# Kernel optimization log

Measured on AMD Instinct MI355X. Metric: run time of the kernel, lower is better.

## Reference

```python
import jax, jax.numpy as jnp
import numpy as np

N = 50000      # nodes
E = 800000     # edges (before self-loops)
H = 2          # attention heads
C = 64         # hidden_channels (per-head out since concat=False)
L = 3          # num_layers - 2 conv blocks
OUT = 128      # readout out_channels
G = 512        # num graphs
VOCAB = 100    # embedding table size
NEG_SLOPE = 0.2


def setup_inputs() -> dict:
    key = jax.random.key(0)
    ks = jax.random.split(key, 12)
    s = 1.0 / np.sqrt(C)
    x = jax.random.randint(ks[0], (N,), 0, VOCAB, dtype=jnp.int32)
    edge_index = jax.random.randint(ks[1], (2, E), 0, N, dtype=jnp.int32)
    batch = jnp.sort(jax.random.randint(ks[2], (N,), 0, G, dtype=jnp.int32))
    embed = jax.random.normal(ks[3], (VOCAB, C), dtype=jnp.float32) * s
    lin_W = jax.random.normal(ks[4], (L, C, C), dtype=jnp.float32) * s
    lin_b = jnp.zeros((L, C), dtype=jnp.float32)
    gat_Wl = jax.random.normal(ks[5], (L, C, H * C), dtype=jnp.float32) * s
    gat_bl = jnp.zeros((L, H * C), dtype=jnp.float32)
    gat_Wr = jax.random.normal(ks[6], (L, C, H * C), dtype=jnp.float32) * s
    gat_br = jnp.zeros((L, H * C), dtype=jnp.float32)
    gat_att = jax.random.normal(ks[7], (L, H, C), dtype=jnp.float32) * s
    gat_bias = jnp.zeros((L, C), dtype=jnp.float32)
    readout_W = jax.random.normal(ks[8], (C, OUT), dtype=jnp.float32) * s
    readout_b = jnp.zeros((OUT,), dtype=jnp.float32)
    return {"x": x, "edge_index": edge_index, "batch": batch, "num_graphs": G,
            "embed": embed, "lin_W": lin_W, "lin_b": lin_b,
            "gat_Wl": gat_Wl, "gat_bl": gat_bl, "gat_Wr": gat_Wr, "gat_br": gat_br,
            "gat_att": gat_att, "gat_bias": gat_bias,
            "readout_W": readout_W, "readout_b": readout_b}


def _gatv2_layer(h, src, dst, Wl, bl, Wr, br, att, bias):
    # lin_l -> source/message features, lin_r -> target features (PyG GATv2Conv)
    xl = (h @ Wl + bl).reshape(N, H, C)
    xr = (h @ Wr + br).reshape(N, H, C)
    # per-edge GATv2 score: a^T LeakyReLU(x_l[j] + x_r[i])
    e = jax.nn.leaky_relu(xl[src] + xr[dst], NEG_SLOPE)      # [E2,H,C]
    score = jnp.einsum('ehc,hc->eh', e, att)                 # [E2,H]
    # segment softmax over incoming edges of each dst node (stable)
    m = jax.lax.stop_gradient(jax.ops.segment_max(score, dst, num_segments=N))
    p = jnp.exp(score - m[dst])
    denom = jax.ops.segment_sum(p, dst, num_segments=N)      # [N,H]
    alpha = p / denom[dst]                                   # [E2,H]
    msg = xl[src] * alpha[:, :, None]                        # [E2,H,C]
    agg = jax.ops.segment_sum(msg, dst, num_segments=N)      # [N,H,C]
    return agg.mean(axis=1) + bias                           # concat=False -> head mean


def reference(x, edge_index, batch, num_graphs, embed, lin_W, lin_b,
              gat_Wl, gat_bl, gat_Wr, gat_br, gat_att, gat_bias,
              readout_W, readout_b):
    # add self loops (GATv2Conv default add_self_loops=True)
    loops = jnp.arange(N, dtype=edge_index.dtype)
    src = jnp.concatenate([edge_index[0], loops])
    dst = jnp.concatenate([edge_index[1], loops])
    h = embed[x]                                             # [N,C]
    for l in range(L):
        h = jax.nn.relu(h @ lin_W[l] + lin_b[l])             # dropout is a no-op in eval
        h = _gatv2_layer(h, src, dst, gat_Wl[l], gat_bl[l], gat_Wr[l], gat_br[l],
                         gat_att[l], gat_bias[l])
    out = h @ readout_W + readout_b                          # [N,OUT]
    return jax.ops.segment_sum(out, batch, num_segments=num_graphs)  # [G,OUT]
```

## Files before the change

### kernel.cpp

```cpp
#include <hip/hip_runtime.h>
#include <hip/hip_fp16.h>

#define N_NODES  50000
#define E_EDGES  800000
#define E_TOT    850000
#define H_HEADS  2
#define C_DIM    64
#define HC       128
#define L_LAYERS 3
#define OUT_DIM  128
#define G_GRAPHS 512
#define NEG_SLOPE 0.2f
#define SCAN_B   196

typedef float v2f __attribute__((ext_vector_type(2)));

__device__ __forceinline__ void lds_fence() { asm volatile("" ::: "memory"); }

__global__ void embed_kernel(const int* __restrict__ x, const float* __restrict__ embed,
                             float* __restrict__ h, int* __restrict__ counts) {
    int i = blockIdx.x * 256 + threadIdx.x;
    if (i < N_NODES) counts[i] = 0;
    if (i >= N_NODES * C_DIM) return;
    int n = i >> 6, c = i & 63;
    h[i] = embed[x[n] * C_DIM + c];
}

__global__ void csr_count_kernel(const int* __restrict__ dsts, int* __restrict__ counts) {
    int e = blockIdx.x * 256 + threadIdx.x;
    if (e >= E_TOT) return;
    int d = (e < E_EDGES) ? dsts[e] : e - E_EDGES;
    atomicAdd(&counts[d], 1);
}

__global__ void scan_partial_kernel(const int* __restrict__ counts, int* __restrict__ row_ptr,
                                    int* __restrict__ partials) {
    __shared__ int wsum[4];
    int i = blockIdx.x * 256 + threadIdx.x;
    int lane = threadIdx.x & 63, wid = threadIdx.x >> 6;
    int cnt = (i < N_NODES) ? counts[i] : 0;
    int v = cnt;
#pragma unroll
    for (int off = 1; off < 64; off <<= 1) {
        int t = __shfl_up(v, off, 64);
        if (lane >= off) v += t;
    }
    if (lane == 63) wsum[wid] = v;
    __syncthreads();
    int woff = 0;
#pragma unroll
    for (int w = 0; w < 4; w++) if (w < wid) woff += wsum[w];
    v += woff;
    if (i < N_NODES) row_ptr[i] = v - cnt;
    if (threadIdx.x == 255) partials[blockIdx.x] = v;
}

__global__ void scan_offsets_kernel(const int* __restrict__ partials, int* __restrict__ block_off) {
    __shared__ int wsum[4];
    int tid = threadIdx.x;
    int lane = tid & 63, wid = tid >> 6;
    int cnt = (tid < SCAN_B) ? partials[tid] : 0;
    int v = cnt;
#pragma unroll
    for (int off = 1; off < 64; off <<= 1) {
        int t = __shfl_up(v, off, 64);
        if (lane >= off) v += t;
    }
    if (lane == 63) wsum[wid] = v;
    __syncthreads();
    int woff = 0;
#pragma unroll
    for (int w = 0; w < 4; w++) if (w < wid) woff += wsum[w];
    v += woff;
    if (tid < SCAN_B) block_off[tid] = v - cnt;
}

__global__ void scan_add_kernel(int* __restrict__ row_ptr, const int* __restrict__ block_off,
                                int* __restrict__ write_off) {
    int i = blockIdx.x * 256 + threadIdx.x;
    if (i < N_NODES) {
        int v = row_ptr[i] + block_off[blockIdx.x];
        row_ptr[i] = v;
        write_off[i] = v;
    }
    if (i == 0) row_ptr[N_NODES] = E_TOT;
}

__global__ void csr_scatter_kernel(const int* __restrict__ srcs, const int* __restrict__ dsts,
                                   int* __restrict__ write_off, int* __restrict__ src_sorted) {
    int e = blockIdx.x * 256 + threadIdx.x;
    if (e >= E_TOT) return;
    int s, d;
    if (e < E_EDGES) { s = srcs[e]; d = dsts[e]; }
    else             { s = d = e - E_EDGES; }
    int pos = atomicAdd(&write_off[d], 1);
    src_sorted[pos] = s;
}

__global__ void layer_lin_kernel(const float* __restrict__ h,
                                 const float* __restrict__ W, const float* __restrict__ b,
                                 const float* __restrict__ Wl, const float* __restrict__ bl,
                                 const float* __restrict__ Wr, const float* __restrict__ br,
                                 __half* __restrict__ xlh, float* __restrict__ xri) {
    __shared__ float sH[16 * 64];
    __shared__ float sH2[16 * 64];
    int tid = threadIdx.x;
    int base = blockIdx.x * 16;
#pragma unroll
    for (int i = 0; i < 4; i++) {
        int idx = tid + i * 256;
        int nn = base + (idx >> 6);
        sH[idx] = (nn < N_NODES) ? h[(size_t)nn * 64 + (idx & 63)] : 0.f;
    }
    __syncthreads();
    {
        int c = tid & 63, g = tid >> 6;
        float a0 = b[c], a1 = a0, a2 = a0, a3 = a0;
        for (int k = 0; k < 64; k++) {
            float wv = W[k * 64 + c];
            a0 = fmaf(sH[(g * 4 + 0) * 64 + k], wv, a0);
            a1 = fmaf(sH[(g * 4 + 1) * 64 + k], wv, a1);
            a2 = fmaf(sH[(g * 4 + 2) * 64 + k], wv, a2);
            a3 = fmaf(sH[(g * 4 + 3) * 64 + k], wv, a3);
        }
        sH2[(g * 4 + 0) * 64 + c] = fmaxf(a0, 0.f);
        sH2[(g * 4 + 1) * 64 + c] = fmaxf(a1, 0.f);
        sH2[(g * 4 + 2) * 64 + c] = fmaxf(a2, 0.f);
        sH2[(g * 4 + 3) * 64 + c] = fmaxf(a3, 0.f);
    }
    __syncthreads();
    {
        int j = tid & 127, gg = tid >> 7;
        float accl[8], accr[8];
#pragma unroll
        for (int n = 0; n < 8; n++) { accl[n] = bl[j]; accr[n] = br[j]; }
        for (int k = 0; k < 64; k++) {
            float wl = Wl[k * 128 + j], wr = Wr[k * 128 + j];
#pragma unroll
            for (int n = 0; n < 8; n++) {
                float hv = sH2[(gg * 8 + n) * 64 + k];
                accl[n] = fmaf(hv, wl, accl[n]);
                accr[n] = fmaf(hv, wr, accr[n]);
            }
        }
        int hh = j >> 6, c = j & 63;
#pragma unroll
        for (int n = 0; n < 8; n++) {
            int node = base + gg * 8 + n;
            if (node < N_NODES) {
                size_t o = (size_t)node * 128 + c * 2 + hh;
                xlh[o] = __float2half(accl[n]);
                xri[o] = accr[n];
            }
        }
    }
}

__global__ void gat_kernel(const __half2* __restrict__ xlh, const float2* __restrict__ xr2,
                           const float* __restrict__ att, const int* __restrict__ row_ptr,
                           const int* __restrict__ src_sorted, const float* __restrict__ bias,
                           float* __restrict__ h_out) {
    __shared__ __align__(16) float cbuf[4][8 * 132];
    int w = threadIdx.x >> 6;
    int d = blockIdx.x * 4 + w;
    if (d >= N_NODES) return;
    int lane = threadIdx.x & 63;
    int r0 = row_ptr[d], r1 = row_ptr[d + 1];
    float2 vrf = xr2[(size_t)d * 64 + lane];
    v2f vr2 = {vrf.x, vrf.y};
    v2f att2 = {att[lane], att[64 + lane]};
    float* cb = cbuf[w];
    int e_of = lane >> 3, p = lane & 7;

    float dpx = 0.f, dpy = 0.f;
    v2f ac0 = {0.f, 0.f}, ac1 = {0.f, 0.f};

#define GAT_LOAD(V, CB) do {                                                    \
        int lim_ = nchunk - 1;                                                  \
        _Pragma("unroll")                                                       \
        for (int e = 0; e < 8; e++) {                                           \
            int ee_ = (CB) + e;                                                 \
            int sv_ = __builtin_amdgcn_readlane(idx, (ee_ < nchunk) ? ee_ : lim_); \
            V[e] = xlh[(size_t)sv_ * 64 + lane];                                \
        }                                                                       \
    } while (0)

#define GAT_PROC(V, CB) do {                                                    \
        int rem_ = nchunk - (CB);                                               \
        v2f vf8[8];                                                             \
        _Pragma("unroll")                                                       \
        for (int e = 0; e < 8; e++) {                                           \
            float2 vf_ = __half22float2(V[e]);                                  \
            v2f vl2 = {vf_.x, vf_.y};                                           \
            vf8[e] = vl2;                                                       \
            v2f z = vl2 + vr2;                                                  \
            v2f t = __builtin_elementwise_max(z, z * NEG_SLOPE) * att2;         \
            *(v2f*)&cb[e * 132 + 2 * lane] = t;                                 \
        }                                                                       \
        lds_fence();                                                            \
        v2f s2 = {0.f, 0.f};                                                    \
        {                                                                       \
            const float4* row_ = (const float4*)&cb[e_of * 132 + p * 16];       \
            _Pragma("unroll")                                                   \
            for (int j = 0; j < 4; j++) {                                       \
                float4 f = row_[j];                                             \
                s2 += (v2f){f.x, f.y};                                          \
                s2 += (v2f){f.z, f.w};                                          \
            }                                                                   \
        }                                                                       \
        lds_fence();                                                            \
        _Pragma("unroll")                                                       \
        for (int off = 1; off <= 4; off <<= 1) {                                \
            v2f o_;                                                             \
            o_.x = __shfl_xor(s2.x, off, 64);                                   \
            o_.y = __shfl_xor(s2.y, off, 64);                                   \
            s2 += o_;                                                           \
        }                                                                       \
        float sx = s2.x, sy = s2.y;                                             \
        if (e_of >= rem_) { sx = -INFINITY; sy = -INFINITY; }                   \
        float wx = __expf(sx), wy = __expf(sy);                                 \
        dpx += wx; dpy += wy;                                                   \
        _Pragma("unroll")                                                       \
        for (int e = 0; e < 8; e++) {                                           \
            float swx = __int_as_float(__builtin_amdgcn_readlane(__float_as_int(wx), 8 * e)); \
            float swy = __int_as_float(__builtin_amdgcn_readlane(__float_as_int(wy), 8 * e)); \
            v2f w2 = {swx, swy};                                                \
            if (e & 1) ac1 = __builtin_elementwise_fma(w2, vf8[e], ac1);        \
            else       ac0 = __builtin_elementwise_fma(w2, vf8[e], ac0);        \
        }                                                                       \
    } while (0)

    for (int base = r0; base < r1; base += 64) {
        int a = base + lane;
        int idx = src_sorted[(a < r1) ? a : (r1 - 1)];
        int nchunk = min(64, r1 - base);
        __half2 va[8], vb[8];
        GAT_LOAD(va, 0);
        int cb_i = 0;
        for (;;) {
            int nx = cb_i + 8;
            if (nx < nchunk) {
                GAT_LOAD(vb, nx);
                GAT_PROC(va, cb_i);
                cb_i = nx;
            } else {
                GAT_PROC(va, cb_i);
                break;
            }
            nx = cb_i + 8;
            if (nx < nchunk) {
                GAT_LOAD(va, nx);
                GAT_PROC(vb, cb_i);
                cb_i = nx;
            } else {
                GAT_PROC(vb, cb_i);
                break;
            }
        }
    }
#undef GAT_LOAD
#undef GAT_PROC

#pragma unroll
    for (int off = 8; off <= 32; off <<= 1) {
        dpx += __shfl_xor(dpx, off, 64);
        dpy += __shfl_xor(dpy, off, 64);
    }
    v2f acc = ac0 + ac1;
    h_out[(size_t)d * 64 + lane] = (acc.x / dpx + acc.y / dpy) * 0.5f + bias[lane];
}

__global__ void zero_out_kernel(float* __restrict__ out) {
    int i = blockIdx.x * 256 + threadIdx.x;
    if (i < G_GRAPHS * OUT_DIM) out[i] = 0.f;
}

__global__ void readout_kernel(const float* __restrict__ h, const float* __restrict__ W,
                               const float* __restrict__ b, const int* __restrict__ batch,
                               float* __restrict__ out) {
    __shared__ float sH[16 * 64];
    __shared__ int sB[16];
    int tid = threadIdx.x;
    int base = blockIdx.x * 16;
#pragma unroll
    for (int i = 0; i < 4; i++) {
        int idx = tid + i * 256;
        int nn = base + (idx >> 6);
        sH[idx] = (nn < N_NODES) ? h[(size_t)nn * 64 + (idx & 63)] : 0.f;
    }
    if (tid < 16) sB[tid] = (base + tid < N_NODES) ? batch[base + tid] : -1;
    __syncthreads();
    int j = tid & 127, gg = tid >> 7;
    float acc[8];
#pragma unroll
    for (int n = 0; n < 8; n++) acc[n] = b[j];
    for (int k = 0; k < 64; k++) {
        float wv = W[k * OUT_DIM + j];
#pragma unroll
        for (int n = 0; n < 8; n++) acc[n] = fmaf(sH[(gg * 8 + n) * 64 + k], wv, acc[n]);
    }
    float run = 0.f; int curb = -2;
#pragma unroll
    for (int n = 0; n < 8; n++) {
        int node = base + gg * 8 + n;
        int bb = (node < N_NODES) ? sB[gg * 8 + n] : -1;
        if (bb != curb) {
            if (curb >= 0) atomicAdd(&out[curb * OUT_DIM + j], run);
            run = 0.f; curb = bb;
        }
        if (bb >= 0) run += acc[n];
    }
    if (curb >= 0) atomicAdd(&out[curb * OUT_DIM + j], run);
}

extern "C" void kernel_launch(void* const* d_in, const int* in_sizes, int n_in,
                              void* d_out, int out_size, void* d_ws, size_t ws_size,
                              hipStream_t stream) {
    const int*   x        = (const int*)d_in[0];
    const int*   edge     = (const int*)d_in[1];
    const int*   batch    = (const int*)d_in[2];
    const float* embed    = (const float*)d_in[4];
    const float* lin_W    = (const float*)d_in[5];
    const float* lin_b    = (const float*)d_in[6];
    const float* gat_Wl   = (const float*)d_in[7];
    const float* gat_bl   = (const float*)d_in[8];
    const float* gat_Wr   = (const float*)d_in[9];
    const float* gat_br   = (const float*)d_in[10];
    const float* gat_att  = (const float*)d_in[11];
    const float* gat_bias = (const float*)d_in[12];
    const float* ro_W     = (const float*)d_in[13];
    const float* ro_b     = (const float*)d_in[14];
    float* out = (float*)d_out;

    const int* srcs = edge;
    const int* dsts = edge + E_EDGES;

    float* h   = (float*)d_ws;
    __half* xlh = (__half*)(h + (size_t)N_NODES * 64);
    float* xr  = (float*)((char*)xlh + (size_t)N_NODES * HC * sizeof(__half));
    int* counts     = (int*)(xr + (size_t)N_NODES * HC);
    int* row_ptr    = counts + N_NODES;
    int* write_off  = row_ptr + N_NODES + 1;
    int* src_sorted = write_off + N_NODES;
    int* partials   = src_sorted + E_TOT;
    int* block_off  = partials + SCAN_B;

    const int T = 256;
    const int gEmbed = (N_NODES * C_DIM + 255) / 256;
    const int gEdge  = (E_TOT + 255) / 256;
    const int gLin   = (N_NODES + 15) / 16;
    const int gGat   = (N_NODES + 3) / 4;
    const int gOut   = (G_GRAPHS * OUT_DIM + 255) / 256;

    embed_kernel<<<gEmbed, T, 0, stream>>>(x, embed, h, counts);

    csr_count_kernel<<<gEdge, T, 0, stream>>>(dsts, counts);
    scan_partial_kernel<<<SCAN_B, T, 0, stream>>>(counts, row_ptr, partials);
    scan_offsets_kernel<<<1, T, 0, stream>>>(partials, block_off);
    scan_add_kernel<<<SCAN_B, T, 0, stream>>>(row_ptr, block_off, write_off);
    csr_scatter_kernel<<<gEdge, T, 0, stream>>>(srcs, dsts, write_off, src_sorted);

    for (int l = 0; l < L_LAYERS; l++) {
        layer_lin_kernel<<<gLin, T, 0, stream>>>(
            h,
            lin_W + (size_t)l * 64 * 64, lin_b + (size_t)l * 64,
            gat_Wl + (size_t)l * 64 * 128, gat_bl + (size_t)l * 128,
            gat_Wr + (size_t)l * 64 * 128, gat_br + (size_t)l * 128,
            xlh, xr);
        gat_kernel<<<gGat, T, 0, stream>>>(
            (const __half2*)xlh, (const float2*)xr, gat_att + (size_t)l * HC,
            row_ptr, src_sorted, gat_bias + (size_t)l * 64, h);
    }

    zero_out_kernel<<<gOut, T, 0, stream>>>(out);
    readout_kernel<<<gLin, T, 0, stream>>>(h, ro_W, ro_b, batch, out);
}
```

Measured before the change: 478.6 us.

## Build CSR via two-pass bucket partition and store sources as 16-bit indices

Replaces the per-edge global atomic scatter into CSR with a two-pass scheme. First, edges are partitioned into 196 buckets of 256 destination nodes using shared-memory histograms and one global atomic per bucket per block. Then each bucket is sorted locally into CSR order with shared atomics. Source indices are stored as unsigned short to halve index traffic in the GAT kernel, but node ids reach 49999 and only fit because that is below 65536; any larger graph would break it. The intent is to cut global atomic contention and scattered writes, at the cost of an extra kernel and an intermediate buffer.

```diff
diff --git a/kernel.cpp b/kernel.cpp
--- a/kernel.cpp
+++ b/kernel.cpp
@@ -12,6 +12,8 @@
 #define G_GRAPHS 512
 #define NEG_SLOPE 0.2f
 #define SCAN_B   196
+#define NB       196
+#define EPB      4096
 
 typedef float v2f __attribute__((ext_vector_type(2)));
 
@@ -76,25 +78,97 @@
 }
 
 __global__ void scan_add_kernel(int* __restrict__ row_ptr, const int* __restrict__ block_off,
-                                int* __restrict__ write_off) {
+                                int* __restrict__ bwptr) {
     int i = blockIdx.x * 256 + threadIdx.x;
     if (i < N_NODES) {
         int v = row_ptr[i] + block_off[blockIdx.x];
         row_ptr[i] = v;
-        write_off[i] = v;
+        if ((i & 255) == 0) bwptr[i >> 8] = v;
     }
     if (i == 0) row_ptr[N_NODES] = E_TOT;
 }
 
-__global__ void csr_scatter_kernel(const int* __restrict__ srcs, const int* __restrict__ dsts,
-                                   int* __restrict__ write_off, int* __restrict__ src_sorted) {
-    int e = blockIdx.x * 256 + threadIdx.x;
-    if (e >= E_TOT) return;
-    int s, d;
-    if (e < E_EDGES) { s = srcs[e]; d = dsts[e]; }
-    else             { s = d = e - E_EDGES; }
-    int pos = atomicAdd(&write_off[d], 1);
-    src_sorted[pos] = s;
+__global__ void edge_partition_kernel(const int* __restrict__ srcs, const int* __restrict__ dsts,
+                                      int* __restrict__ bwptr, unsigned int* __restrict__ ebuf) {
+    __shared__ int hist[256];
+    __shared__ int lscan[256];
+    __shared__ int sExcl[256];
+    __shared__ int lcnt[256];
+    __shared__ int gbase[256];
+    __shared__ unsigned int sval[EPB];
+    __shared__ unsigned char sgid[EPB];
+    int tid = threadIdx.x;
+    int ebase = blockIdx.x * EPB;
+    hist[tid] = 0;
+    __syncthreads();
+    unsigned int val[16];
+    int gid[16];
+#pragma unroll
+    for (int i = 0; i < 16; i++) {
+        int e = ebase + i * 256 + tid;
+        if (e < E_TOT) {
+            int s, d;
+            if (e < E_EDGES) { s = srcs[e]; d = dsts[e]; }
+            else             { s = d = e - E_EDGES; }
+            val[i] = ((unsigned)s << 8) | (unsigned)(d & 255);
+            gid[i] = d >> 8;
+            atomicAdd(&hist[gid[i]], 1);
+        } else gid[i] = -1;
+    }
+    __syncthreads();
+    lscan[tid] = hist[tid];
+    __syncthreads();
+#pragma unroll
+    for (int off = 1; off < 256; off <<= 1) {
+        int t = (tid >= off) ? lscan[tid - off] : 0;
+        __syncthreads();
+        lscan[tid] += t;
+        __syncthreads();
+    }
+    sExcl[tid] = lscan[tid] - hist[tid];
+    lcnt[tid] = 0;
+    __syncthreads();
+#pragma unroll
+    for (int i = 0; i < 16; i++) {
+        if (gid[i] >= 0) {
+            int off = atomicAdd(&lcnt[gid[i]], 1);
+            int idx = sExcl[gid[i]] + off;
+            sval[idx] = val[i];
+            sgid[idx] = (unsigned char)gid[i];
+        }
+    }
+    if (tid < NB) {
+        int c = hist[tid];
+        gbase[tid] = c ? atomicAdd(&bwptr[tid], c) : 0;
+    }
+    __syncthreads();
+    int total = lscan[255];
+    for (int idx = tid; idx < total; idx += 256) {
+        int g = sgid[idx];
+        ebuf[gbase[g] + (idx - sExcl[g])] = sval[idx];
+    }
+}
+
+__global__ void bucket_csr_kernel(const unsigned int* __restrict__ ebuf,
+                                  const int* __restrict__ row_ptr,
+                                  unsigned short* __restrict__ src_sorted) {
+    __shared__ int lbase[256];
+    __shared__ int lcnt[256];
+    int g = blockIdx.x, tid = threadIdx.x;
+    int n0 = g << 8;
+    int nodes = min(256, N_NODES - n0);
+    int b0 = row_ptr[n0];
+    int b1 = row_ptr[min(n0 + 256, N_NODES)];
+    if (tid < nodes) lbase[tid] = row_ptr[n0 + tid] - b0;
+    lcnt[tid] = 0;
+    __syncthreads();
+    int cnt = b1 - b0;
+    for (int i = tid; i < cnt; i += 256) {
+        unsigned int v = ebuf[b0 + i];
+        int dl = v & 255;
+        int slot = lbase[dl] + atomicAdd(&lcnt[dl], 1);
+        src_sorted[b0 + slot] = (unsigned short)(v >> 8);
+    }
 }
 
 __global__ void layer_lin_kernel(const float* __restrict__ h,
@@ -158,7 +232,8 @@
 
 __global__ void gat_kernel(const __half2* __restrict__ xlh, const float2* __restrict__ xr2,
                            const float* __restrict__ att, const int* __restrict__ row_ptr,
-                           const int* __restrict__ src_sorted, const float* __restrict__ bias,
+                           const unsigned short* __restrict__ src_sorted,
+                           const float* __restrict__ bias,
                            float* __restrict__ h_out) {
     __shared__ __align__(16) float cbuf[4][8 * 132];
     int w = threadIdx.x >> 6;
@@ -232,7 +307,7 @@
 
     for (int base = r0; base < r1; base += 64) {
         int a = base + lane;
-        int idx = src_sorted[(a < r1) ? a : (r1 - 1)];
+        int idx = (int)src_sorted[(a < r1) ? a : (r1 - 1)];
         int nchunk = min(64, r1 - base);
         __half2 va[8], vb[8];
         GAT_LOAD(va, 0);
@@ -335,19 +410,21 @@
     const int* srcs = edge;
     const int* dsts = edge + E_EDGES;
 
-    float* h   = (float*)d_ws;
+    float* h    = (float*)d_ws;
     __half* xlh = (__half*)(h + (size_t)N_NODES * 64);
-    float* xr  = (float*)((char*)xlh + (size_t)N_NODES * HC * sizeof(__half));
+    float* xr   = (float*)((char*)xlh + (size_t)N_NODES * HC * sizeof(__half));
     int* counts     = (int*)(xr + (size_t)N_NODES * HC);
     int* row_ptr    = counts + N_NODES;
-    int* write_off  = row_ptr + N_NODES + 1;
-    int* src_sorted = write_off + N_NODES;
-    int* partials   = src_sorted + E_TOT;
+    int* bwptr      = row_ptr + N_NODES + 1;
+    int* partials   = bwptr + 256;
     int* block_off  = partials + SCAN_B;
+    unsigned int* ebuf = (unsigned int*)(block_off + SCAN_B);
+    unsigned short* src_sorted = (unsigned short*)(ebuf + E_TOT);
 
     const int T = 256;
     const int gEmbed = (N_NODES * C_DIM + 255) / 256;
     const int gEdge  = (E_TOT + 255) / 256;
+    const int gPart  = (E_TOT + EPB - 1) / EPB;
     const int gLin   = (N_NODES + 15) / 16;
     const int gGat   = (N_NODES + 3) / 4;
     const int gOut   = (G_GRAPHS * OUT_DIM + 255) / 256;
@@ -357,8 +434,9 @@
     csr_count_kernel<<<gEdge, T, 0, stream>>>(dsts, counts);
     scan_partial_kernel<<<SCAN_B, T, 0, stream>>>(counts, row_ptr, partials);
     scan_offsets_kernel<<<1, T, 0, stream>>>(partials, block_off);
-    scan_add_kernel<<<SCAN_B, T, 0, stream>>>(row_ptr, block_off, write_off);
-    csr_scatter_kernel<<<gEdge, T, 0, stream>>>(srcs, dsts, write_off, src_sorted);
+    scan_add_kernel<<<SCAN_B, T, 0, stream>>>(row_ptr, block_off, bwptr);
+    edge_partition_kernel<<<gPart, T, 0, stream>>>(srcs, dsts, bwptr, ebuf);
+    bucket_csr_kernel<<<NB, T, 0, stream>>>(ebuf, row_ptr, src_sorted);
 
     for (int l = 0; l < L_LAYERS; l++) {
         layer_lin_kernel<<<gLin, T, 0, stream>>>(
```

After: 451.9 us. -5.6%, faster.
